# Performance work log

Hardware: AMD Instinct MI355X
Metric: run time of the kernel (lower is better)

Reference implementation:

```python
import jax, jax.numpy as jnp
import numpy as np

N = 100000      # nodes
E = 1600000     # edges (avg degree 16)
EMB = 64        # embedding_size (per-head out channels)
H = 2           # heads (hardcoded in module)
HID = 128       # hidden_size
NEG_SLOPE = 0.2 # GATv2 default


def setup_inputs() -> dict:
    key = jax.random.key(0)
    ks = jax.random.split(key, 12)
    s = 0.1
    x = jax.random.normal(ks[0], (N, 1), jnp.float32)
    edge_index = jax.random.randint(ks[1], (2, E), 0, N, dtype=jnp.int64)
    edge_attr = jax.random.normal(ks[2], (E, 1), jnp.float32)
    # GATv2Conv params (in_channels=1, out=EMB, heads=H, edge_dim=1)
    W_l = jax.random.normal(ks[3], (1, H * EMB), jnp.float32) * s
    b_l = jnp.zeros((H * EMB,), jnp.float32)
    W_r = jax.random.normal(ks[4], (1, H * EMB), jnp.float32) * s
    b_r = jnp.zeros((H * EMB,), jnp.float32)
    W_e = jax.random.normal(ks[5], (1, H * EMB), jnp.float32) * s   # lin_edge, bias=False
    att = jax.random.normal(ks[6], (H, EMB), jnp.float32) * s       # attention vector a
    bias_out = jnp.zeros((H * EMB,), jnp.float32)                   # conv output bias (concat=True)
    # fc: Linear(embedding_size*4, hidden_size)
    W_fc = jax.random.normal(ks[7], (HID, 4 * EMB), jnp.float32) * s
    b_fc = jnp.zeros((HID,), jnp.float32)
    return {
        "x": x, "edge_index": edge_index, "edge_attr": edge_attr,
        "target_node_idx": 123,
        "W_l": W_l, "b_l": b_l, "W_r": W_r, "b_r": b_r,
        "W_e": W_e, "att": att, "bias_out": bias_out,
        "W_fc": W_fc, "b_fc": b_fc,
    }


def reference(x, edge_index, edge_attr, target_node_idx,
              W_l, b_l, W_r, b_r, W_e, att, bias_out, W_fc, b_fc):
    n = x.shape[0]
    h, c = att.shape
    src, dst = edge_index[0], edge_index[1]

    # add_self_loops with fill_value='mean': per-target-node mean of incoming edge_attr
    deg = jax.ops.segment_sum(jnp.ones((src.shape[0],), x.dtype), dst, num_segments=n)
    attr_mean = jax.ops.segment_sum(edge_attr, dst, num_segments=n) / jnp.maximum(deg, 1.0)[:, None]
    loop = jnp.arange(n, dtype=src.dtype)
    src_f = jnp.concatenate([src, loop])
    dst_f = jnp.concatenate([dst, loop])
    ea = jnp.concatenate([edge_attr, attr_mean], axis=0)  # [E+N, 1]

    # per-head node transforms
    x_l = (x @ W_l + b_l).reshape(n, h, c)  # source transform
    x_r = (x @ W_r + b_r).reshape(n, h, c)  # target transform
    e_edge = (ea @ W_e).reshape(-1, h, c)   # edge-feature transform

    # GATv2: e_ij = a^T LeakyReLU(W_l x_j + W_r x_i + W_e e_ij)
    e = jax.nn.leaky_relu(x_l[src_f] + x_r[dst_f] + e_edge, NEG_SLOPE)  # [E', H, C]
    logits = jnp.einsum('ehc,hc->eh', e, att)  # [E', H]

    # segment softmax over incoming edges per target node
    m = jax.ops.segment_max(logits, dst_f, num_segments=n)     # [N, H]
    expv = jnp.exp(logits - m[dst_f])
    denom = jax.ops.segment_sum(expv, dst_f, num_segments=n)
    alpha = expv / denom[dst_f]                                 # [E', H]

    # weighted scatter-aggregate of source messages, concat heads, add bias
    out = jax.ops.segment_sum(alpha[:, :, None] * x_l[src_f], dst_f, num_segments=n)
    graph_emb = out.reshape(n, h * c) + bias_out                # [N, 2*EMB]

    # gather target, repeat, concat, linear
    tgt = graph_emb[target_node_idx]                            # [2*EMB]
    combined = jnp.concatenate([graph_emb, jnp.broadcast_to(tgt[None, :], graph_emb.shape)], axis=1)
    return combined @ W_fc.T + b_fc                             # [N, HID]
```

## Files before the change

### kernel.cpp

```cpp
#include <hip/hip_runtime.h>
#include <math.h>


#define LRELU_A1 0.6f
#define LRELU_A2 0.4f
#define TB       256
#define EPB      1024
#define NE       (EPB / TB)
#define NPB      128
#define NB_MAX   1024
#define SW       512

__global__ void k_prep(const unsigned int* __restrict__ ei,
                       const float* __restrict__ att,
                       const float* __restrict__ W_l,
                       const float* __restrict__ b_l, const float* __restrict__ b_r,
                       const float* __restrict__ bias_out,
                       const float* __restrict__ W_fc, const float* __restrict__ b_fc,
                       float* __restrict__ C) {
  int j = threadIdx.x;
  unsigned long long nz = __ballot(j < 32 && ei[2 * j + 1] != 0u);
  if (j == 0) ((int*)C)[1024] = (nz == 0ull) ? 1 : 0;
  if (j >= 128) return;
  float a = att[j];
  C[j] = LRELU_A1 * a;
  C[128 + j] = LRELU_A2 * a;
  C[256 + j] = b_l[j] + b_r[j];
  const float* wrow = W_fc + j * 256;
  float u0 = 0.f, u1 = 0.f, v0 = 0.f, v1 = 0.f, cb = b_fc[j];
  for (int c = 0; c < 64; c++) {
    u0 = fmaf(W_l[c],      wrow[c],       u0);
    u1 = fmaf(W_l[64 + c], wrow[64 + c],  u1);
    v0 = fmaf(W_l[c],      wrow[128 + c], v0);
    v1 = fmaf(W_l[64 + c], wrow[192 + c], v1);
  }
  for (int t = 0; t < 128; t++) {
    float gb = b_l[t] + bias_out[t];
    cb = fmaf(gb, wrow[t] + wrow[128 + t], cb);
  }
  C[384 + j] = u0;
  C[512 + j] = u1;
  C[640 + j] = v0;
  C[768 + j] = v1;
  C[896 + j] = cb;
}

#define CH_STEP(comp, ACC, i)                                                      \
  do {                                                                             \
    float v_ = fmaf(xs8[i], wl.comp, fmaf(xt8[i], wr.comp, fmaf(ae8[i], we.comp, bb.comp))); \
    ACC[i] = fmaf(a2.comp, fabsf(v_), fmaf(a1.comp, v_, ACC[i]));                  \
  } while (0)

__global__ __launch_bounds__(TB, 4) void k_bin(
    const float* __restrict__ x, const int* __restrict__ ei,
    const float* __restrict__ ea,
    const float* __restrict__ WL, const float* __restrict__ WR,
    const float* __restrict__ WE, const float* __restrict__ C,
    int4* __restrict__ rec, int* __restrict__ offsT,
    int NB, int S_BLOCKS, int E) {
  __shared__ int cnt[NB_MAX];
  __shared__ int pfx[NB_MAX + 1];
  __shared__ int wsum[4];
  const int tid = threadIdx.x;
  for (int i = tid; i < NB_MAX; i += TB) cnt[i] = 0;
  __syncthreads();

  const int e0 = blockIdx.x * EPB;
  const bool w64 = ((const int*)C)[1024] != 0;
  const float* A1 = C;
  const float* A2 = C + 128;
  const float* BASE = C + 256;

  int de8[NE];
  float ae8[NE], xs8[NE], xt8[NE];
  bool ok[NE];
#pragma unroll
  for (int i = 0; i < NE; i++) {
    int e = e0 + i * TB + tid;
    ok[i] = (e < E);
    int ee = ok[i] ? e : 0;
    int s_ = w64 ? ei[2 * ee] : ei[ee];
    int d_ = w64 ? ei[2 * (E + ee)] : ei[E + ee];
    de8[i] = d_;
    ae8[i] = ea[ee];
    xs8[i] = x[s_];
    xt8[i] = x[d_];
  }
  float acc0[NE], acc1[NE];
#pragma unroll
  for (int i = 0; i < NE; i++) { acc0[i] = 0.f; acc1[i] = 0.f; }
#pragma unroll 2
  for (int jb = 0; jb < 64; jb += 4) {
    float4 wl = *(const float4*)(WL + jb);
    float4 wr = *(const float4*)(WR + jb);
    float4 we = *(const float4*)(WE + jb);
    float4 bb = *(const float4*)(BASE + jb);
    float4 a1 = *(const float4*)(A1 + jb);
    float4 a2 = *(const float4*)(A2 + jb);
#pragma unroll
    for (int i = 0; i < NE; i++) {
      CH_STEP(x, acc0, i); CH_STEP(y, acc0, i); CH_STEP(z, acc0, i); CH_STEP(w, acc0, i);
    }
  }
#pragma unroll 2
  for (int jb = 64; jb < 128; jb += 4) {
    float4 wl = *(const float4*)(WL + jb);
    float4 wr = *(const float4*)(WR + jb);
    float4 we = *(const float4*)(WE + jb);
    float4 bb = *(const float4*)(BASE + jb);
    float4 a1 = *(const float4*)(A1 + jb);
    float4 a2 = *(const float4*)(A2 + jb);
#pragma unroll
    for (int i = 0; i < NE; i++) {
      CH_STEP(x, acc1, i); CH_STEP(y, acc1, i); CH_STEP(z, acc1, i); CH_STEP(w, acc1, i);
    }
  }
  int b8[NE], slot8[NE], p0[NE], p1[NE], p2[NE], p3[NE];
#pragma unroll
  for (int i = 0; i < NE; i++) {
    int d_ = de8[i];
    b8[i] = d_ >> 7;
    p0[i] = __float_as_int(__expf(acc0[i]));
    p1[i] = __float_as_int(__expf(acc1[i]));
    p2[i] = __float_as_int(xs8[i]);
    p3[i] = (int)((__float_as_uint(ae8[i]) & ~127u) | (unsigned)(d_ & 127));
    slot8[i] = ok[i] ? atomicAdd(&cnt[b8[i]], 1) : 0;
  }
  __syncthreads();
  int l4[4], mysum = 0;
#pragma unroll
  for (int j = 0; j < 4; j++) {
    int idx = tid * 4 + j;
    l4[j] = (idx < NB) ? cnt[idx] : 0;
    mysum += l4[j];
  }
  const int lane = tid & 63, wv = tid >> 6;
  int inc = mysum;
#pragma unroll
  for (int d = 1; d < 64; d <<= 1) {
    int t = __shfl_up(inc, d);
    if (lane >= d) inc += t;
  }
  if (lane == 63) wsum[wv] = inc;
  __syncthreads();
  int wbase = 0;
#pragma unroll
  for (int w = 0; w < 4; w++) if (w < wv) wbase += wsum[w];
  int run = wbase + inc - mysum;
#pragma unroll
  for (int j = 0; j < 4; j++) {
    int idx = tid * 4 + j;
    if (idx < NB) { pfx[idx] = run; run += l4[j]; }
  }
  if (tid == 0) pfx[NB] = wsum[0] + wsum[1] + wsum[2] + wsum[3];
  __syncthreads();
  for (int b = tid; b <= NB; b += TB)
    offsT[(size_t)b * S_BLOCKS + blockIdx.x] = pfx[b];
  int4* myrec = rec + (size_t)blockIdx.x * EPB;
#pragma unroll
  for (int i = 0; i < NE; i++) {
    if (ok[i]) myrec[pfx[b8[i]] + slot8[i]] = make_int4(p0[i], p1[i], p2[i], p3[i]);
  }
}

__global__ __launch_bounds__(TB, 4) void k_reduce(
    const int4* __restrict__ rec, const int* __restrict__ offsT,
    float* __restrict__ Spart, int S_BLOCKS, int SPP) {
  __shared__ int4 sorted[SW];
  __shared__ int lut[SW];
  __shared__ int cnt[NPB];
  __shared__ int pos0[NPB];
  __shared__ int claim[NPB];
  __shared__ int wsum[4];
  const int tid = threadIdx.x;
  const int b = blockIdx.x;
  const int part = blockIdx.y;

  const int sA = part * SPP + tid;
  const int sB = sA + TB;
  int stA = 0, lenA = 0, stB = 0, lenB = 0;
  if (tid < SPP && sA < S_BLOCKS) {
    stA  = offsT[(size_t)b * S_BLOCKS + sA];
    lenA = offsT[(size_t)(b + 1) * S_BLOCKS + sA] - stA;
  }
  if (TB + tid < SPP && sB < S_BLOCKS) {
    stB  = offsT[(size_t)b * S_BLOCKS + sB];
    lenB = offsT[(size_t)(b + 1) * S_BLOCKS + sB] - stB;
  }
  const int rbA = sA * EPB + stA;
  const int rbB = sB * EPB + stB;
  const int mysum = lenA + lenB;
  if (tid < NPB) cnt[tid] = 0;
  const int lane = tid & 63, wv = tid >> 6;
  int inc = mysum;
#pragma unroll
  for (int d = 1; d < 64; d <<= 1) {
    int t = __shfl_up(inc, d);
    if (lane >= d) inc += t;
  }
  if (lane == 63) wsum[wv] = inc;
  __syncthreads();
  int wbase = 0;
#pragma unroll
  for (int w = 0; w < 4; w++) if (w < wv) wbase += wsum[w];
  const int T = wsum[0] + wsum[1] + wsum[2] + wsum[3];
  const int bsA = wbase + inc - mysum;
  const int bsB = bsA + lenA;

  float r0 = 0.f, r1 = 0.f, r2 = 0.f, r3 = 0.f, r4 = 0.f;
  int rc = 0;

  for (int w0 = 0; w0 < T; w0 += SW) {
    const int w1 = min(w0 + SW, T);
    {
      int lo = max(bsA, w0), hi = min(bsA + lenA, w1);
      for (int k = lo; k < hi; k++) lut[k - w0] = rbA + (k - bsA);
      lo = max(bsB, w0); hi = min(bsB + lenB, w1);
      for (int k = lo; k < hi; k++) lut[k - w0] = rbB + (k - bsB);
    }
    __syncthreads();
    for (int i = w0 + tid; i < w1; i += TB) {
      int4 r = rec[(size_t)(unsigned)lut[i - w0]];
      atomicAdd(&cnt[(int)((unsigned)r.w & 127u)], 1);
    }
    __syncthreads();
    if (tid < 64) {
      int c0 = cnt[2 * tid], c1 = cnt[2 * tid + 1];
      int s = c0 + c1;
      for (int d = 1; d < 64; d <<= 1) {
        int t = __shfl_up(s, d);
        if (tid >= d) s += t;
      }
      int excl = s - (c0 + c1);
      pos0[2 * tid] = excl;
      pos0[2 * tid + 1] = excl + c0;
      claim[2 * tid] = excl;
      claim[2 * tid + 1] = excl + c0;
    }
    __syncthreads();
    for (int i = w0 + tid; i < w1; i += TB) {
      int4 r = rec[(size_t)(unsigned)lut[i - w0]];
      int node = (int)((unsigned)r.w & 127u);
      int slot = atomicAdd(&claim[node], 1);
      sorted[slot] = r;
    }
    __syncthreads();
    if (tid < NPB) {
      int p = pos0[tid], c = cnt[tid];
      for (int k = 0; k < c; k++) {
        int4 r = sorted[p + k];
        float e0v = __int_as_float(r.x);
        float e1v = __int_as_float(r.y);
        float xsv = __int_as_float(r.z);
        float aev = __uint_as_float((unsigned)r.w & ~127u);
        r0 += e0v;
        r1 += e0v * xsv;
        r2 += e1v;
        r3 += e1v * xsv;
        r4 += aev;
      }
      rc += c;
      cnt[tid] = 0;
    }
    __syncthreads();
  }
  if (tid < NPB) {
    float* out = Spart + ((size_t)b * gridDim.y + part) * (NPB * 6) + tid * 6;
    out[0] = r0; out[1] = r1; out[2] = r2;
    out[3] = r3; out[4] = r4; out[5] = (float)rc;
  }
}

__global__ __launch_bounds__(256) void k_fin(
    const float* __restrict__ x,
    const float* __restrict__ WL, const float* __restrict__ WR,
    const float* __restrict__ WE, const float* __restrict__ C,
    const float* __restrict__ Spart, float* __restrict__ S,
    int N, int P) {
  int n = blockIdx.x * blockDim.x + threadIdx.x;
  if (n >= N) return;
  int b = n >> 7, t = n & 127;
  const float* q0 = Spart + ((size_t)b * P) * (NPB * 6) + t * 6;
  float den0 = 0.f, num0 = 0.f, den1 = 0.f, num1 = 0.f, asum = 0.f, cntv = 0.f;
  for (int p = 0; p < P; p++) {
    const float* q = q0 + (size_t)p * (NPB * 6);
    float2 v0 = *(const float2*)(q);
    float2 v1 = *(const float2*)(q + 2);
    float2 v2 = *(const float2*)(q + 4);
    den0 += v0.x; num0 += v0.y;
    den1 += v1.x; num1 += v1.y;
    asum += v2.x; cntv += v2.y;
  }
  const float* A1 = C;
  const float* A2 = C + 128;
  const float* BASE = C + 256;
  float xn = x[n];
  float am = asum / fmaxf(cntv, 1.0f);
  float acc0 = 0.f, acc1 = 0.f;
#pragma unroll 4
  for (int jb = 0; jb < 64; jb += 4) {
    float4 wl = *(const float4*)(WL + jb);
    float4 wr = *(const float4*)(WR + jb);
    float4 we = *(const float4*)(WE + jb);
    float4 bb = *(const float4*)(BASE + jb);
    float4 a1 = *(const float4*)(A1 + jb);
    float4 a2 = *(const float4*)(A2 + jb);
    float v;
    v = fmaf(xn, wl.x + wr.x, fmaf(am, we.x, bb.x)); acc0 = fmaf(a2.x, fabsf(v), fmaf(a1.x, v, acc0));
    v = fmaf(xn, wl.y + wr.y, fmaf(am, we.y, bb.y)); acc0 = fmaf(a2.y, fabsf(v), fmaf(a1.y, v, acc0));
    v = fmaf(xn, wl.z + wr.z, fmaf(am, we.z, bb.z)); acc0 = fmaf(a2.z, fabsf(v), fmaf(a1.z, v, acc0));
    v = fmaf(xn, wl.w + wr.w, fmaf(am, we.w, bb.w)); acc0 = fmaf(a2.w, fabsf(v), fmaf(a1.w, v, acc0));
  }
#pragma unroll 4
  for (int jb = 64; jb < 128; jb += 4) {
    float4 wl = *(const float4*)(WL + jb);
    float4 wr = *(const float4*)(WR + jb);
    float4 we = *(const float4*)(WE + jb);
    float4 bb = *(const float4*)(BASE + jb);
    float4 a1 = *(const float4*)(A1 + jb);
    float4 a2 = *(const float4*)(A2 + jb);
    float v;
    v = fmaf(xn, wl.x + wr.x, fmaf(am, we.x, bb.x)); acc1 = fmaf(a2.x, fabsf(v), fmaf(a1.x, v, acc1));
    v = fmaf(xn, wl.y + wr.y, fmaf(am, we.y, bb.y)); acc1 = fmaf(a2.y, fabsf(v), fmaf(a1.y, v, acc1));
    v = fmaf(xn, wl.z + wr.z, fmaf(am, we.z, bb.z)); acc1 = fmaf(a2.z, fabsf(v), fmaf(a1.z, v, acc1));
    v = fmaf(xn, wl.w + wr.w, fmaf(am, we.w, bb.w)); acc1 = fmaf(a2.w, fabsf(v), fmaf(a1.w, v, acc1));
  }
  float s0 = __expf(acc0), s1 = __expf(acc1);
  float2 sv;
  sv.x = (num0 + s0 * xn) / (den0 + s0);
  sv.y = (num1 + s1 * xn) / (den1 + s1);
  *(float2*)(S + 2 * n) = sv;
}

__global__ __launch_bounds__(256) void k_out(
    const float* __restrict__ S, const float* __restrict__ C,
    const int* __restrict__ tgtp, float* __restrict__ out, int N) {
  int g = blockIdx.x * blockDim.x + threadIdx.x;
  if (g >= N * 32) return;
  int n = g >> 5;
  int kq = (g & 31) * 4;
  int T = tgtp[0];
  float s0t = S[2 * T], s1t = S[2 * T + 1];
  float2 s = *(const float2*)(S + 2 * n);
  float4 u0 = *(const float4*)(C + 384 + kq);
  float4 u1 = *(const float4*)(C + 512 + kq);
  float4 v0 = *(const float4*)(C + 640 + kq);
  float4 v1 = *(const float4*)(C + 768 + kq);
  float4 cb = *(const float4*)(C + 896 + kq);
  float4 o;
  o.x = fmaf(s.x, u0.x, fmaf(s.y, u1.x, fmaf(s0t, v0.x, fmaf(s1t, v1.x, cb.x))));
  o.y = fmaf(s.x, u0.y, fmaf(s.y, u1.y, fmaf(s0t, v0.y, fmaf(s1t, v1.y, cb.y))));
  o.z = fmaf(s.x, u0.z, fmaf(s.y, u1.z, fmaf(s0t, v0.z, fmaf(s1t, v1.z, cb.z))));
  o.w = fmaf(s.x, u0.w, fmaf(s.y, u1.w, fmaf(s0t, v0.w, fmaf(s1t, v1.w, cb.w))));
  *(float4*)(out + n * 128 + kq) = o;
}

extern "C" void kernel_launch(void* const* d_in, const int* in_sizes, int n_in,
                              void* d_out, int out_size, void* d_ws, size_t ws_size,
                              hipStream_t stream) {
  const float* x        = (const float*)d_in[0];
  const int*   ei       = (const int*)d_in[1];
  const float* ea       = (const float*)d_in[2];
  const int*   tgt      = (const int*)d_in[3];
  const float* W_l      = (const float*)d_in[4];
  const float* b_l      = (const float*)d_in[5];
  const float* W_r      = (const float*)d_in[6];
  const float* b_r      = (const float*)d_in[7];
  const float* W_e      = (const float*)d_in[8];
  const float* att      = (const float*)d_in[9];
  const float* bias_out = (const float*)d_in[10];
  const float* W_fc     = (const float*)d_in[11];
  const float* b_fc     = (const float*)d_in[12];

  const int N = in_sizes[0];
  const int E = in_sizes[2];
  const int NB = (N + NPB - 1) / NPB;
  const int S_BLOCKS = (E + EPB - 1) / EPB;

  const size_t sz_rec  = (size_t)S_BLOCKS * EPB * 16;
  const size_t sz_offs = (size_t)(NB + 1) * S_BLOCKS * 4;
  const size_t sz_S    = (size_t)2 * N * 4;
  const size_t sz_C    = 4608;
  int P = 8;
  while (P > 2 &&
         sz_rec + sz_offs + sz_S + sz_C + (size_t)NB * P * NPB * 6 * 4 > ws_size)
    P >>= 1;
  const int SPP = (S_BLOCKS + P - 1) / P;

  char* p = (char*)d_ws;
  int4*  rec   = (int4*)p;                      p += sz_rec;
  int*   offsT = (int*)p;                       p += sz_offs;
  float* S     = (float*)p;                     p += sz_S;
  float* C     = (float*)p;                     p += sz_C;
  float* Spart = (float*)p;

  k_prep<<<1, 128, 0, stream>>>((const unsigned int*)ei, att, W_l, b_l, b_r,
                                bias_out, W_fc, b_fc, C);
  k_bin<<<S_BLOCKS, TB, 0, stream>>>(x, ei, ea, W_l, W_r, W_e, C,
                                     rec, offsT, NB, S_BLOCKS, E);
  k_reduce<<<dim3(NB, P), TB, 0, stream>>>(rec, offsT, Spart, S_BLOCKS, SPP);
  k_fin<<<(N + 255) / 256, 256, 0, stream>>>(x, W_l, W_r, W_e, C, Spart, S, N, P);
  k_out<<<(N * 32 + 255) / 256, 256, 0, stream>>>(S, C, tgt, (float*)d_out, N);
}
```

Measured before the change: 206.3 us.

## Write bin offsets row-major and transpose them in a separate tiled kernel

The binning kernel used to write its per-bin prefix offsets strided by S_BLOCKS, which produced scattered uncoalesced stores. It now writes each block's offsets contiguously, and a new shared-memory tiled transpose kernel builds the bin-major layout that the reduce kernel reads. The LDS atomic slot claims are also moved ahead of the attention math so their latency can overlap it, and the channel loops are fully unrolled. In exchange this adds a kernel launch, an extra buffer and an extra pass over the offset arrays, and full unrolling may raise register pressure.

```diff
diff --git a/kernel.cpp b/kernel.cpp
--- a/kernel.cpp
+++ b/kernel.cpp
@@ -10,6 +10,7 @@
 #define NPB      128
 #define NB_MAX   1024
 #define SW       512
+#define TSZ      32
 
 __global__ void k_prep(const unsigned int* __restrict__ ei,
                        const float* __restrict__ att,
@@ -56,7 +57,7 @@
     const float* __restrict__ ea,
     const float* __restrict__ WL, const float* __restrict__ WR,
     const float* __restrict__ WE, const float* __restrict__ C,
-    int4* __restrict__ rec, int* __restrict__ offsT,
+    int4* __restrict__ rec, int* __restrict__ offs,
     int NB, int S_BLOCKS, int E) {
   __shared__ int cnt[NB_MAX];
   __shared__ int pfx[NB_MAX + 1];
@@ -86,10 +87,16 @@
     xs8[i] = x[s_];
     xt8[i] = x[d_];
   }
+  int b8[NE], slot8[NE];
+#pragma unroll
+  for (int i = 0; i < NE; i++) {
+    b8[i] = de8[i] >> 7;
+    slot8[i] = ok[i] ? atomicAdd(&cnt[b8[i]], 1) : 0;
+  }
   float acc0[NE], acc1[NE];
 #pragma unroll
   for (int i = 0; i < NE; i++) { acc0[i] = 0.f; acc1[i] = 0.f; }
-#pragma unroll 2
+#pragma unroll
   for (int jb = 0; jb < 64; jb += 4) {
     float4 wl = *(const float4*)(WL + jb);
     float4 wr = *(const float4*)(WR + jb);
@@ -102,7 +109,7 @@
       CH_STEP(x, acc0, i); CH_STEP(y, acc0, i); CH_STEP(z, acc0, i); CH_STEP(w, acc0, i);
     }
   }
-#pragma unroll 2
+#pragma unroll
   for (int jb = 64; jb < 128; jb += 4) {
     float4 wl = *(const float4*)(WL + jb);
     float4 wr = *(const float4*)(WR + jb);
@@ -115,16 +122,13 @@
       CH_STEP(x, acc1, i); CH_STEP(y, acc1, i); CH_STEP(z, acc1, i); CH_STEP(w, acc1, i);
     }
   }
-  int b8[NE], slot8[NE], p0[NE], p1[NE], p2[NE], p3[NE];
+  int p0[NE], p1[NE], p2[NE], p3[NE];
 #pragma unroll
   for (int i = 0; i < NE; i++) {
-    int d_ = de8[i];
-    b8[i] = d_ >> 7;
     p0[i] = __float_as_int(__expf(acc0[i]));
     p1[i] = __float_as_int(__expf(acc1[i]));
     p2[i] = __float_as_int(xs8[i]);
-    p3[i] = (int)((__float_as_uint(ae8[i]) & ~127u) | (unsigned)(d_ & 127));
-    slot8[i] = ok[i] ? atomicAdd(&cnt[b8[i]], 1) : 0;
+    p3[i] = (int)((__float_as_uint(ae8[i]) & ~127u) | (unsigned)(de8[i] & 127));
   }
   __syncthreads();
   int l4[4], mysum = 0;
@@ -154,12 +158,30 @@
   }
   if (tid == 0) pfx[NB] = wsum[0] + wsum[1] + wsum[2] + wsum[3];
   __syncthreads();
-  for (int b = tid; b <= NB; b += TB)
-    offsT[(size_t)b * S_BLOCKS + blockIdx.x] = pfx[b];
+  int* myoffs = offs + (size_t)blockIdx.x * (NB + 1);
+  for (int b = tid; b <= NB; b += TB) myoffs[b] = pfx[b];
   int4* myrec = rec + (size_t)blockIdx.x * EPB;
 #pragma unroll
   for (int i = 0; i < NE; i++) {
     if (ok[i]) myrec[pfx[b8[i]] + slot8[i]] = make_int4(p0[i], p1[i], p2[i], p3[i]);
+  }
+}
+
+__global__ __launch_bounds__(256) void k_xpose(const int* __restrict__ offs,
+                                               int* __restrict__ offsT,
+                                               int R, int SB) {
+  __shared__ int tile[TSZ][TSZ + 1];
+  const int b0 = blockIdx.x * TSZ;
+  const int s0 = blockIdx.y * TSZ;
+  const int tx = threadIdx.x & 31, ty = threadIdx.x >> 5;
+  for (int i = ty; i < TSZ; i += 8) {
+    int s = s0 + i, b = b0 + tx;
+    tile[i][tx] = (s < SB && b < R) ? offs[(size_t)s * R + b] : 0;
+  }
+  __syncthreads();
+  for (int i = ty; i < TSZ; i += 8) {
+    int b = b0 + i, s = s0 + tx;
+    if (b < R && s < SB) offsT[(size_t)b * SB + s] = tile[tx][i];
   }
 }
 
@@ -377,19 +399,22 @@
   const int NB = (N + NPB - 1) / NPB;
   const int S_BLOCKS = (E + EPB - 1) / EPB;
 
-  const size_t sz_rec  = (size_t)S_BLOCKS * EPB * 16;
-  const size_t sz_offs = (size_t)(NB + 1) * S_BLOCKS * 4;
-  const size_t sz_S    = (size_t)2 * N * 4;
-  const size_t sz_C    = 4608;
+  const size_t sz_rec   = (size_t)S_BLOCKS * EPB * 16;
+  const size_t sz_offs  = (size_t)S_BLOCKS * (NB + 1) * 4;
+  const size_t sz_offsT = (size_t)(NB + 1) * S_BLOCKS * 4;
+  const size_t sz_S     = (size_t)2 * N * 4;
+  const size_t sz_C     = 4608;
   int P = 8;
   while (P > 2 &&
-         sz_rec + sz_offs + sz_S + sz_C + (size_t)NB * P * NPB * 6 * 4 > ws_size)
+         sz_rec + sz_offs + sz_offsT + sz_S + sz_C +
+             (size_t)NB * P * NPB * 6 * 4 > ws_size)
     P >>= 1;
   const int SPP = (S_BLOCKS + P - 1) / P;
 
   char* p = (char*)d_ws;
   int4*  rec   = (int4*)p;                      p += sz_rec;
-  int*   offsT = (int*)p;                       p += sz_offs;
+  int*   offs  = (int*)p;                       p += sz_offs;
+  int*   offsT = (int*)p;                       p += sz_offsT;
   float* S     = (float*)p;                     p += sz_S;
   float* C     = (float*)p;                     p += sz_C;
   float* Spart = (float*)p;
@@ -397,7 +422,9 @@
   k_prep<<<1, 128, 0, stream>>>((const unsigned int*)ei, att, W_l, b_l, b_r,
                                 bias_out, W_fc, b_fc, C);
   k_bin<<<S_BLOCKS, TB, 0, stream>>>(x, ei, ea, W_l, W_r, W_e, C,
-                                     rec, offsT, NB, S_BLOCKS, E);
+                                     rec, offs, NB, S_BLOCKS, E);
+  k_xpose<<<dim3((NB + 1 + TSZ - 1) / TSZ, (S_BLOCKS + TSZ - 1) / TSZ),
+            256, 0, stream>>>(offs, offsT, NB + 1, S_BLOCKS);
   k_reduce<<<dim3(NB, P), TB, 0, stream>>>(rec, offsT, Spart, S_BLOCKS, SPP);
   k_fin<<<(N + 255) / 256, 256, 0, stream>>>(x, W_l, W_r, W_e, C, Spart, S, N, P);
   k_out<<<(N * 32 + 255) / 256, 256, 0, stream>>>(S, C, tgt, (float*)d_out, N);
```

Result: slower. 534.9 us (+159.2%).
